# Performance work log

Measured on AMD Instinct MI355X. Metric: run time of the kernel, lower is better.

Reference implementation:

```python
import jax, jax.numpy as jnp
import numpy as np

B, L, D, FF = 4, 4096, 1024, 4096
EPS = 1e-06


def setup_inputs() -> dict:
    key = jax.random.key(0)
    ks = jax.random.split(key, 20)
    s_d = 1.0 / np.sqrt(D)
    s_ff = 1.0 / np.sqrt(FF)
    inp = {
        "x": jax.random.normal(ks[0], (B, L, D), jnp.float32),
        "hidden": jax.random.normal(ks[1], (B, D), jnp.float32),
        # sioconv linears (stored as [in, out])
        "w_ln_z": jax.random.normal(ks[2], (D, D), jnp.float32) * s_d,
        "b_ln_z": jnp.zeros((D,), jnp.float32),
        "w_dt": jax.random.normal(ks[3], (D, D), jnp.float32) * s_d,
        "b_dt": jnp.zeros((D,), jnp.float32),
        "w_y": jax.random.normal(ks[4], (D, D), jnp.float32) * s_d,
        "b_y": jnp.zeros((D,), jnp.float32),
        "w_y_act": jax.random.normal(ks[5], (D, D), jnp.float32) * s_d,
        "b_y_act": jnp.zeros((D,), jnp.float32),
        # FFN SwiGLU
        "w_fc": jax.random.normal(ks[6], (D, FF), jnp.float32) * s_d,
        "b_fc": jnp.zeros((FF,), jnp.float32),
        "w_fc_act": jax.random.normal(ks[7], (D, FF), jnp.float32) * s_d,
        "b_fc_act": jnp.zeros((FF,), jnp.float32),
        "w_out": jax.random.normal(ks[8], (FF, D), jnp.float32) * s_ff,
        "b_out": jnp.zeros((D,), jnp.float32),
        # RMSNorm gains
        "g_sio": jnp.ones((D,), jnp.float32),
        "g_ffn": jnp.ones((D,), jnp.float32),
    }
    return inp


def _rmsnorm(x, g):
    return x * jax.lax.rsqrt(jnp.mean(x * x, axis=-1, keepdims=True) + EPS) * g


def _sioconv(x, hidden, w_ln_z, b_ln_z, w_dt, b_dt, w_y, b_y, w_y_act, b_y_act):
    # x: [B,L,D], hidden: [B,D]
    ln_z = -jax.nn.softplus(-(x @ w_ln_z + b_ln_z))       # [B,L,D]
    dt = x @ w_dt + b_dt
    ln_da = -jax.nn.softplus(-dt)
    ln_o_da = -jax.nn.softplus(dt)
    ln_o_da_cumsum = jnp.cumsum(ln_o_da, axis=1)
    # inner-chunk: exp(logcumsumexp(ln_z + ln_da - cumsum) + cumsum)
    lse = jax.lax.cumlogsumexp(ln_z + ln_da - ln_o_da_cumsum, axis=1)
    h_inner = jnp.exp(lse + ln_o_da_cumsum)
    # cross-chunk: decay applied to incoming hidden state
    h_cross = jnp.exp(ln_o_da_cumsum) * hidden[:, None, :]
    h = h_inner + h_cross
    y = (h @ w_y + b_y) * jax.nn.silu(x @ w_y_act + b_y_act)
    return y, h


def _ffn(x, w_fc, b_fc, w_fc_act, b_fc_act, w_out, b_out):
    return (x @ w_fc + b_fc) * jax.nn.silu(x @ w_fc_act + b_fc_act) @ w_out + b_out


def reference(x, hidden, w_ln_z, b_ln_z, w_dt, b_dt, w_y, b_y, w_y_act, b_y_act,
              w_fc, b_fc, w_fc_act, b_fc_act, w_out, b_out, g_sio, g_ffn):
    x_res = x
    y, h = _sioconv(_rmsnorm(x, g_sio), hidden,
                    w_ln_z, b_ln_z, w_dt, b_dt, w_y, b_y, w_y_act, b_y_act)
    x = y + x_res  # dropout is identity (p=0 / eval)
    x_res = x
    x = _ffn(_rmsnorm(x, g_ffn), w_fc, b_fc, w_fc_act, b_fc_act, w_out, b_out) + x_res
    return (x, h)
```

## Files before the change

kernel.cpp:

```cpp
#include <hip/hip_runtime.h>
#include <stdint.h>

using u16 = unsigned short;
typedef __attribute__((ext_vector_type(8))) __bf16 bf16x8;
typedef __attribute__((ext_vector_type(4))) float f32x4;

#define DEV __device__ __forceinline__

static constexpr int kB = 4, kL = 4096, kD = 1024, kFF = 4096;
static constexpr int kM = kB * kL;
static constexpr int kLC = 256, kNC = kL / kLC;
static constexpr float kEPS = 1e-6f;

DEV u16 f2bf(float v) {
  union { float f; uint32_t u; } x; x.f = v;
  uint32_t r = x.u + 0x7FFFu + ((x.u >> 16) & 1u);
  return (u16)(r >> 16);
}
DEV float bf2f(u16 u) {
  union { uint32_t u; float f; } x; x.u = (uint32_t)u << 16; return x.f;
}
DEV float sigm(float x) { return 1.0f / (1.0f + __expf(-x)); }

DEV void gload_lds16(const void* g, void* l) {
  __builtin_amdgcn_global_load_lds(
      (const __attribute__((address_space(1))) void*)g,
      (__attribute__((address_space(3))) void*)l, 16, 0, 0);
}

__global__ __launch_bounds__(256) void wtrans_all(
    const float* __restrict__ w_ln_z, const float* __restrict__ w_dt,
    const float* __restrict__ w_fca, const float* __restrict__ w_fc,
    const float* __restrict__ w_yact, const float* __restrict__ w_y,
    const float* __restrict__ w_out_,
    u16* __restrict__ wzdT, u16* __restrict__ wfgT, u16* __restrict__ wyaT,
    u16* __restrict__ wyT, u16* __restrict__ woutT) {
  const int bid = blockIdx.x;
  const float *a, *b; u16* out; int K, Ncols, bx, local; bool pair;
  if (bid < 2048)       { local = bid;         a = w_ln_z; b = w_dt; out = wzdT;  K = 1024; Ncols = 1024; bx = 64;  pair = true;  }
  else if (bid < 10240) { local = bid - 2048;  a = w_fca;  b = w_fc; out = wfgT;  K = 1024; Ncols = 4096; bx = 256; pair = true;  }
  else if (bid < 11264) { local = bid - 10240; a = w_yact; b = nullptr; out = wyaT; K = 1024; Ncols = 1024; bx = 32; pair = false; }
  else if (bid < 12288) { local = bid - 11264; a = w_y;    b = nullptr; out = wyT;  K = 1024; Ncols = 1024; bx = 32; pair = false; }
  else                  { local = bid - 12288; a = w_out_; b = nullptr; out = woutT; K = 4096; Ncols = 1024; bx = 32; pair = false; }
  const int n0 = (local % bx) * 32, k0 = (local / bx) * 32;
  __shared__ float t[32][33];
  const int tx = threadIdx.x, ty = threadIdx.y;
  const float* src; int c0;
  if (pair) { src = ((n0 >> 5) & 1) ? b : a; c0 = (n0 >> 6) * 32; }
  else      { src = a; c0 = n0; }
#pragma unroll
  for (int i = 0; i < 4; ++i)
    t[ty + i * 8][tx] = src[(size_t)(k0 + ty + i * 8) * Ncols + (c0 + tx)];
  __syncthreads();
#pragma unroll
  for (int i = 0; i < 4; ++i)
    out[(size_t)(n0 + ty + i * 8) * K + (k0 + tx)] = f2bf(t[tx][ty + i * 8]);
}

__global__ __launch_bounds__(256) void rmsnorm_kernel(const float* __restrict__ x,
                                                      const float* __restrict__ g,
                                                      u16* __restrict__ out) {
  const int row = blockIdx.x;
  const int t = threadIdx.x;
  const float4 v = ((const float4*)(x + (size_t)row * kD))[t];
  float ss = v.x * v.x + v.y * v.y + v.z * v.z + v.w * v.w;
#pragma unroll
  for (int o = 1; o < 64; o <<= 1) ss += __shfl_xor(ss, o, 64);
  __shared__ float red[4];
  if ((t & 63) == 0) red[t >> 6] = ss;
  __syncthreads();
  const float tot = red[0] + red[1] + red[2] + red[3];
  const float sc = rsqrtf(tot * (1.0f / kD) + kEPS);
  const float4 gv = ((const float4*)g)[t];
  const uint32_t lo = (uint32_t)f2bf(v.x * sc * gv.x) | ((uint32_t)f2bf(v.y * sc * gv.y) << 16);
  const uint32_t hi = (uint32_t)f2bf(v.z * sc * gv.z) | ((uint32_t)f2bf(v.w * sc * gv.w) << 16);
  *(uint2*)(out + (size_t)row * kD + t * 4) = make_uint2(lo, hi);
}

template <int MODE>
__global__ __launch_bounds__(512) void gemm256(
    const u16* __restrict__ A, const u16* __restrict__ Bt,
    const float* __restrict__ bias, const float* __restrict__ bias2,
    const u16* __restrict__ aux, int auxld,
    const float* __restrict__ res, float* __restrict__ Cf,
    u16* __restrict__ Cb, u16* __restrict__ C2b,
    int M, int N, int K) {
  __shared__ u16 sm[65536];
  const int tid = threadIdx.x;
  const int lane = tid & 63;
  const int wave = tid >> 6;
  const int wr = wave >> 2, wc = wave & 3;

  const int gx = gridDim.x;
  const int nwg = gx * gridDim.y;
  const int bid = blockIdx.y * gx + blockIdx.x;
  const int q = nwg >> 3, r = nwg & 7;
  const int xcd = bid & 7, idx0 = bid >> 3;
  const int wg = (xcd < r ? xcd * (q + 1) : r * (q + 1) + (xcd - r) * q) + idx0;
  const int m0 = (wg / gx) * 256, n0 = (wg % gx) * 256;

  const int NK = K >> 6;

  const int l8 = lane >> 3, l7 = lane & 7;
  const int rsub = wave * 8 + l8;
  const int kel = (l7 ^ l8) * 8;
  const size_t srcA = (size_t)(m0 + rsub) * K + kel;
  const size_t srcB = (size_t)(n0 + rsub) * K + kel;

  auto stage_half = [&](int kt, int half) {
    const int bsel = (kt & 1) * 32768;
    if (half < 2) {
      u16* d = sm + bsel + tid * 8 + half * 8192;
      const u16* s = A + srcA + (size_t)kt * 64 + (size_t)(half * 2) * 64 * K;
      gload_lds16(s, d);
      gload_lds16(s + (size_t)64 * K, d + 4096);
    } else {
      const int hh = half - 2;
      u16* d = sm + bsel + 16384 + tid * 8 + hh * 8192;
      const u16* s = Bt + srcB + (size_t)kt * 64 + (size_t)(hh * 2) * 64 * K;
      gload_lds16(s, d);
      gload_lds16(s + (size_t)64 * K, d + 4096);
    }
  };

  const int ra = lane & 15;
  const int kx0 = ((lane >> 4) ^ l7) * 8;
  const int kx1 = (((lane >> 4) + 4) ^ l7) * 8;

  f32x4 acc[8][4] = {};
  bf16x8 al[4][2], ah[4][2], bl[2][2], bh[2][2];

  stage_half(0, 0); stage_half(0, 1); stage_half(0, 2); stage_half(0, 3);
  stage_half(1, 0);
  asm volatile("s_waitcnt vmcnt(2)");
  asm volatile("s_barrier" ::: "memory");

  for (int h = 0; h < NK; ++h) {
    const u16* as = sm + (h & 1) * 32768 + (wr * 128 + ra) * 64;
    const u16* bs = sm + (h & 1) * 32768 + 16384 + (wc * 64 + ra) * 64;

#pragma unroll
    for (int mi = 0; mi < 4; ++mi) {
      al[mi][0] = *(const bf16x8*)(as + mi * 16 * 64 + kx0);
      al[mi][1] = *(const bf16x8*)(as + mi * 16 * 64 + kx1);
    }
#pragma unroll
    for (int ni = 0; ni < 2; ++ni) {
      bl[ni][0] = *(const bf16x8*)(bs + ni * 16 * 64 + kx0);
      bl[ni][1] = *(const bf16x8*)(bs + ni * 16 * 64 + kx1);
    }
    if (h + 1 < NK) stage_half(h + 1, 1);
    asm volatile("s_barrier" ::: "memory");
    asm volatile("s_waitcnt lgkmcnt(0)");
    __builtin_amdgcn_s_setprio(1);
#pragma unroll
    for (int mi = 0; mi < 4; ++mi)
#pragma unroll
      for (int ni = 0; ni < 2; ++ni)
#pragma unroll
        for (int kk = 0; kk < 2; ++kk)
          acc[mi][ni] = __builtin_amdgcn_mfma_f32_16x16x32_bf16(al[mi][kk], bl[ni][kk], acc[mi][ni], 0, 0, 0);
    __builtin_amdgcn_s_setprio(0);
    asm volatile("s_barrier" ::: "memory");

#pragma unroll
    for (int ni = 0; ni < 2; ++ni) {
      bh[ni][0] = *(const bf16x8*)(bs + (32 + ni * 16) * 64 + kx0);
      bh[ni][1] = *(const bf16x8*)(bs + (32 + ni * 16) * 64 + kx1);
    }
    if (h + 1 < NK) stage_half(h + 1, 2);
    asm volatile("s_barrier" ::: "memory");
    asm volatile("s_waitcnt lgkmcnt(0)");
    __builtin_amdgcn_s_setprio(1);
#pragma unroll
    for (int mi = 0; mi < 4; ++mi)
#pragma unroll
      for (int ni = 0; ni < 2; ++ni)
#pragma unroll
        for (int kk = 0; kk < 2; ++kk)
          acc[mi][2 + ni] = __builtin_amdgcn_mfma_f32_16x16x32_bf16(al[mi][kk], bh[ni][kk], acc[mi][2 + ni], 0, 0, 0);
    __builtin_amdgcn_s_setprio(0);
    asm volatile("s_barrier" ::: "memory");

#pragma unroll
    for (int mi = 0; mi < 4; ++mi) {
      ah[mi][0] = *(const bf16x8*)(as + (64 + mi * 16) * 64 + kx0);
      ah[mi][1] = *(const bf16x8*)(as + (64 + mi * 16) * 64 + kx1);
    }
    if (h + 1 < NK) stage_half(h + 1, 3);
    asm volatile("s_barrier" ::: "memory");
    asm volatile("s_waitcnt lgkmcnt(0)");
    __builtin_amdgcn_s_setprio(1);
#pragma unroll
    for (int mi = 0; mi < 4; ++mi)
#pragma unroll
      for (int ni = 0; ni < 2; ++ni)
#pragma unroll
        for (int kk = 0; kk < 2; ++kk)
          acc[4 + mi][ni] = __builtin_amdgcn_mfma_f32_16x16x32_bf16(ah[mi][kk], bl[ni][kk], acc[4 + mi][ni], 0, 0, 0);
    __builtin_amdgcn_s_setprio(0);
    asm volatile("s_barrier" ::: "memory");

    if (h + 2 < NK) stage_half(h + 2, 0);
    asm volatile("s_barrier" ::: "memory");
    __builtin_amdgcn_s_setprio(1);
#pragma unroll
    for (int mi = 0; mi < 4; ++mi)
#pragma unroll
      for (int ni = 0; ni < 2; ++ni)
#pragma unroll
        for (int kk = 0; kk < 2; ++kk)
          acc[4 + mi][2 + ni] = __builtin_amdgcn_mfma_f32_16x16x32_bf16(ah[mi][kk], bh[ni][kk], acc[4 + mi][2 + ni], 0, 0, 0);
    __builtin_amdgcn_s_setprio(0);
    if (h + 2 < NK) asm volatile("s_waitcnt vmcnt(2)");
    else            asm volatile("s_waitcnt vmcnt(0)");
    asm volatile("s_barrier" ::: "memory");
  }

  const int ca = ra;
  const int rq = (lane >> 4) * 4;
  if (MODE == 7) {
    const int Nout = N >> 1;
#pragma unroll
    for (int mi = 0; mi < 8; ++mi) {
#pragma unroll
      for (int ni = 0; ni < 2; ++ni) {
        const int cout = (n0 >> 1) + wc * 32 + ni * 16 + ca;
        const float b1 = bias[cout], b2 = bias2[cout];
#pragma unroll
        for (int j = 0; j < 4; ++j) {
          const int rr = m0 + wr * 128 + mi * 16 + rq + j;
          const size_t idx = (size_t)rr * Nout + cout;
          const float v1 = acc[mi][ni][j] + b1;
          const float v2 = acc[mi][2 + ni][j] + b2;
          Cf[idx] = sigm(-v2);
          C2b[idx] = f2bf(sigm(v1) * sigm(v2));
        }
      }
    }
  } else {
#pragma unroll
    for (int mi = 0; mi < 8; ++mi) {
#pragma unroll
      for (int ni = 0; ni < 4; ++ni) {
        const int c = n0 + wc * 64 + ni * 16 + ca;
        const float bz = bias[c];
#pragma unroll
        for (int j = 0; j < 4; ++j) {
          const int rr = m0 + wr * 128 + mi * 16 + rq + j;
          const size_t idx = (size_t)rr * N + c;
          const float v = acc[mi][ni][j] + bz;
          if (MODE == 2) {
            const float a = bf2f(aux[(size_t)rr * auxld + c]);
            Cf[idx] = v * (a * sigm(a)) + res[idx];
          } else if (MODE == 4) {
            Cf[idx] = v + res[idx];
          } else {
            Cb[idx] = f2bf(v);
          }
        }
      }
    }
  }
}

__global__ __launch_bounds__(512, 4) void gemm_ffn(
    const u16* __restrict__ A, const u16* __restrict__ Bt,
    const float* __restrict__ bias, const float* __restrict__ bias2,
    u16* __restrict__ Cb, int M, int N, int K) {
  __shared__ u16 sm[24576];
  const int tid = threadIdx.x;
  const int lane = tid & 63;
  const int wave = tid >> 6;
  const int wr = wave >> 1, wc = wave & 1;

  const int gx = gridDim.x;
  const int nwg = gx * gridDim.y;
  const int bid = blockIdx.y * gx + blockIdx.x;
  const int q = nwg >> 3, r = nwg & 7;
  const int xcd = bid & 7, idx0 = bid >> 3;
  const int wg = (xcd < r ? xcd * (q + 1) : r * (q + 1) + (xcd - r) * q) + idx0;
  const int per = gridDim.y * 4;
  const int sg = wg / per, srem = wg % per;
  const int m0 = (srem >> 2) * 256;
  const int n0 = (sg * 4 + (srem & 3)) * 128;

  const int NK = K >> 5;

  const int rsub = wave * 16 + (lane >> 2);
  const int kel = ((lane & 3) ^ ((lane >> 3) & 3)) * 8;
  const size_t srcA = (size_t)(m0 + rsub) * K + kel;
  const size_t srcB = (size_t)(n0 + rsub) * K + kel;

  auto stageA = [&](int kt) {
    u16* d = sm + (kt & 1) * 12288 + tid * 8;
    const u16* s = A + srcA + (size_t)kt * 32;
    gload_lds16(s, d);
    gload_lds16(s + (size_t)128 * K, d + 4096);
  };
  auto stageB = [&](int kt) {
    gload_lds16(Bt + srcB + (size_t)kt * 32,
                sm + (kt & 1) * 12288 + 8192 + tid * 8);
  };

  const int ra = lane & 15;
  const int rb = ra * 32 + ((((lane >> 4) ^ (ra >> 1)) & 3) << 3);

  f32x4 acc[4][4] = {};
  bf16x8 af[4], bfr[4];

  stageA(0); stageB(0);
  if (NK > 1) { stageA(1); stageB(1); }
  asm volatile("s_waitcnt vmcnt(3)");
  asm volatile("s_barrier" ::: "memory");

  for (int h = 0; h < NK; ++h) {
    const u16* Az = sm + (h & 1) * 12288 + wr * 2048;
    const u16* Bz = sm + (h & 1) * 12288 + 8192 + wc * 2048;

#pragma unroll
    for (int mi = 0; mi < 4; ++mi) af[mi] = *(const bf16x8*)(Az + mi * 512 + rb);
    bfr[0] = *(const bf16x8*)(Bz + rb);
    bfr[1] = *(const bf16x8*)(Bz + 512 + rb);
    asm volatile("s_barrier" ::: "memory");
    asm volatile("s_waitcnt lgkmcnt(0)");
    __builtin_amdgcn_s_setprio(1);
#pragma unroll
    for (int mi = 0; mi < 4; ++mi)
#pragma unroll
      for (int ni = 0; ni < 2; ++ni)
        acc[mi][ni] = __builtin_amdgcn_mfma_f32_16x16x32_bf16(af[mi], bfr[ni], acc[mi][ni], 0, 0, 0);
    __builtin_amdgcn_s_setprio(0);
    asm volatile("s_barrier" ::: "memory");

    bfr[2] = *(const bf16x8*)(Bz + 1024 + rb);
    bfr[3] = *(const bf16x8*)(Bz + 1536 + rb);
    if (h + 2 < NK) stageA(h + 2);
    asm volatile("s_barrier" ::: "memory");
    asm volatile("s_waitcnt lgkmcnt(0)");
    __builtin_amdgcn_s_setprio(1);
#pragma unroll
    for (int mi = 0; mi < 4; ++mi)
      acc[mi][2] = __builtin_amdgcn_mfma_f32_16x16x32_bf16(af[mi], bfr[2], acc[mi][2], 0, 0, 0);
    __builtin_amdgcn_s_setprio(0);
    asm volatile("s_barrier" ::: "memory");

    if (h + 2 < NK) stageB(h + 2);
    __builtin_amdgcn_s_setprio(1);
#pragma unroll
    for (int mi = 0; mi < 4; ++mi)
      acc[mi][3] = __builtin_amdgcn_mfma_f32_16x16x32_bf16(af[mi], bfr[3], acc[mi][3], 0, 0, 0);
    __builtin_amdgcn_s_setprio(0);
    if (h + 2 < NK) asm volatile("s_waitcnt vmcnt(3)");
    else            asm volatile("s_waitcnt vmcnt(0)");
    asm volatile("s_barrier" ::: "memory");
  }

  const int ca = lane & 15;
  const int rq = (lane >> 4) * 4;
  const int Nout = N >> 1;
#pragma unroll
  for (int mi = 0; mi < 4; ++mi) {
#pragma unroll
    for (int ni = 0; ni < 2; ++ni) {
      const int cout = (n0 >> 1) + wc * 32 + ni * 16 + ca;
      const float b1 = bias[cout], b2 = bias2[cout];
#pragma unroll
      for (int j = 0; j < 4; ++j) {
        const int rr = m0 + wr * 64 + mi * 16 + rq + j;
        const size_t idx = (size_t)rr * Nout + cout;
        const float v1 = acc[mi][ni][j] + b1;
        const float v2 = acc[mi][2 + ni][j] + b2;
        Cb[idx] = f2bf(v2 * (v1 * sigm(v1)));
      }
    }
  }
}

__global__ __launch_bounds__(256) void scan_phase1(const float* __restrict__ Aa,
                                                   const u16* __restrict__ Bv,
                                                   float* __restrict__ P,
                                                   float* __restrict__ S) {
  const int d = blockIdx.x * 256 + threadIdx.x;
  const int c = blockIdx.y, b = blockIdx.z;
  size_t base = ((size_t)b * kL + (size_t)c * kLC) * kD + d;
  float p = 1.0f, s = 0.0f;
#pragma unroll 4
  for (int l = 0; l < kLC; ++l) {
    const float a = Aa[base];
    const float bv = bf2f(Bv[base]);
    p *= a;
    s = fmaf(a, s, bv);
    base += kD;
  }
  const size_t o = ((size_t)b * kNC + c) * kD + d;
  P[o] = p; S[o] = s;
}

__global__ __launch_bounds__(256) void scan_phase2(const float* __restrict__ P,
                                                   const float* __restrict__ S,
                                                   const float* __restrict__ hidden,
                                                   float* __restrict__ Hini) {
  const int d = blockIdx.x * 256 + threadIdx.x;
  const int b = blockIdx.y;
  float carry = hidden[(size_t)b * kD + d];
  for (int c = 0; c < kNC; ++c) {
    const size_t o = ((size_t)b * kNC + c) * kD + d;
    Hini[o] = carry;
    carry = fmaf(P[o], carry, S[o]);
  }
}

__global__ __launch_bounds__(256) void scan_phase3(const float* __restrict__ Aa,
                                                   const u16* __restrict__ Bv,
                                                   const float* __restrict__ Hini,
                                                   float* __restrict__ Hout,
                                                   u16* __restrict__ Hbf) {
  const int d = blockIdx.x * 256 + threadIdx.x;
  const int c = blockIdx.y, b = blockIdx.z;
  float h = Hini[((size_t)b * kNC + c) * kD + d];
  size_t base = ((size_t)b * kL + (size_t)c * kLC) * kD + d;
#pragma unroll 4
  for (int l = 0; l < kLC; ++l) {
    h = fmaf(Aa[base], h, bf2f(Bv[base]));
    Hout[base] = h;
    Hbf[base] = f2bf(h);
    base += kD;
  }
}

extern "C" void kernel_launch(void* const* d_in, const int* in_sizes, int n_in,
                              void* d_out, int out_size, void* d_ws, size_t ws_size,
                              hipStream_t stream) {
  const float* x      = (const float*)d_in[0];
  const float* hidden = (const float*)d_in[1];
  const float* w_ln_z = (const float*)d_in[2];
  const float* b_ln_z = (const float*)d_in[3];
  const float* w_dt   = (const float*)d_in[4];
  const float* b_dt   = (const float*)d_in[5];
  const float* w_y    = (const float*)d_in[6];
  const float* b_y    = (const float*)d_in[7];
  const float* w_yact = (const float*)d_in[8];
  const float* b_yact = (const float*)d_in[9];
  const float* w_fc   = (const float*)d_in[10];
  const float* b_fc   = (const float*)d_in[11];
  const float* w_fca  = (const float*)d_in[12];
  const float* b_fca  = (const float*)d_in[13];
  const float* w_out  = (const float*)d_in[14];
  const float* b_out  = (const float*)d_in[15];
  const float* g_sio  = (const float*)d_in[16];
  const float* g_ffn  = (const float*)d_in[17];

  char* ws = (char*)d_ws;
  const size_t MiB = 1ull << 20;
  u16* wzdT  = (u16*)(ws + 0 * MiB);
  u16* wyaT  = (u16*)(ws + 4 * MiB);
  u16* wyT   = (u16*)(ws + 6 * MiB);
  u16* wfgT  = (u16*)(ws + 8 * MiB);
  u16* woutT = (u16*)(ws + 24 * MiB);
  u16*   xn    = (u16*)(ws + 33 * MiB);
  u16*   yabuf = (u16*)(ws + 65 * MiB);
  float* Abuf  = (float*)(ws + 97 * MiB);
  u16*   Bvbuf = (u16*)(ws + 161 * MiB);
  u16*   hbf   = (u16*)(ws + 225 * MiB);
  u16*   Ubuf  = (u16*)(ws + 161 * MiB);
  float* Pbuf  = (float*)(ws + 289 * MiB);
  float* Sbuf  = (float*)(ws + 290 * MiB);
  float* Hini  = (float*)(ws + 291 * MiB);

  float* xout = (float*)d_out;
  float* hout = xout + (size_t)kM * kD;
  float* x1 = Abuf;

  wtrans_all<<<16384, dim3(32, 8), 0, stream>>>(
      w_ln_z, w_dt, w_fca, w_fc, w_yact, w_y, w_out,
      wzdT, wfgT, wyaT, wyT, woutT);

  rmsnorm_kernel<<<kM, 256, 0, stream>>>(x, g_sio, xn);

  gemm256<7><<<dim3(2048 / 256, kM / 256), 512, 0, stream>>>(
      xn, wzdT, b_ln_z, b_dt, nullptr, 0, nullptr, Abuf, nullptr, Bvbuf, kM, 2048, kD);
  gemm256<5><<<dim3(kD / 256, kM / 256), 512, 0, stream>>>(
      xn, wyaT, b_yact, nullptr, nullptr, 0, nullptr, nullptr, yabuf, nullptr, kM, kD, kD);

  scan_phase1<<<dim3(kD / 256, kNC, kB), 256, 0, stream>>>(Abuf, Bvbuf, Pbuf, Sbuf);
  scan_phase2<<<dim3(kD / 256, kB), 256, 0, stream>>>(Pbuf, Sbuf, hidden, Hini);
  scan_phase3<<<dim3(kD / 256, kNC, kB), 256, 0, stream>>>(Abuf, Bvbuf, Hini, hout, hbf);

  gemm256<2><<<dim3(kD / 256, kM / 256), 512, 0, stream>>>(
      hbf, wyT, b_y, nullptr, yabuf, kD, x, x1, nullptr, nullptr, kM, kD, kD);

  rmsnorm_kernel<<<kM, 256, 0, stream>>>(x1, g_ffn, xn);

  gemm_ffn<<<dim3(8192 / 128, kM / 256), 512, 0, stream>>>(
      xn, wfgT, b_fca, b_fc, Ubuf, kM, 8192, kD);

  gemm256<4><<<dim3(kD / 256, kM / 256), 512, 0, stream>>>(
      Ubuf, woutT, b_out, nullptr, nullptr, 0, x1, xout, nullptr, nullptr, kM, kD, kFF);
}
```

Baseline: 732.5 us.

## Fuse scan chunk reduction into gate GEMM epilogue and store residual in bf16

The per-chunk product/sum reduction of the scan (scan_phase1) now runs inside the MODE 7 GEMM epilogue, using shuffles and shared memory across the 256-row tile, so the separate pass that re-read the A and B buffers is gone. Separately, the intermediate residual x1 is written as bf16 instead of fp32. The second RMSNorm and the final output GEMM read that bf16 copy, which cuts memory traffic. The cost is lower precision on the residual path and a longer GEMM epilogue. The fused reduction also relies on each 256-row tile lining up exactly with one scan chunk.

```diff
diff --git a/kernel.cpp b/kernel.cpp
--- a/kernel.cpp
+++ b/kernel.cpp
@@ -77,6 +77,28 @@
   *(uint2*)(out + (size_t)row * kD + t * 4) = make_uint2(lo, hi);
 }
 
+__global__ __launch_bounds__(256) void rmsnorm_b16(const u16* __restrict__ x,
+                                                   const float* __restrict__ g,
+                                                   u16* __restrict__ out) {
+  const int row = blockIdx.x;
+  const int t = threadIdx.x;
+  const uint2 raw = ((const uint2*)(x + (size_t)row * kD))[t];
+  const float v0 = bf2f((u16)(raw.x & 0xffff)), v1 = bf2f((u16)(raw.x >> 16));
+  const float v2 = bf2f((u16)(raw.y & 0xffff)), v3 = bf2f((u16)(raw.y >> 16));
+  float ss = v0 * v0 + v1 * v1 + v2 * v2 + v3 * v3;
+#pragma unroll
+  for (int o = 1; o < 64; o <<= 1) ss += __shfl_xor(ss, o, 64);
+  __shared__ float red[4];
+  if ((t & 63) == 0) red[t >> 6] = ss;
+  __syncthreads();
+  const float tot = red[0] + red[1] + red[2] + red[3];
+  const float sc = rsqrtf(tot * (1.0f / kD) + kEPS);
+  const float4 gv = ((const float4*)g)[t];
+  const uint32_t lo = (uint32_t)f2bf(v0 * sc * gv.x) | ((uint32_t)f2bf(v1 * sc * gv.y) << 16);
+  const uint32_t hi = (uint32_t)f2bf(v2 * sc * gv.z) | ((uint32_t)f2bf(v3 * sc * gv.w) << 16);
+  *(uint2*)(out + (size_t)row * kD + t * 4) = make_uint2(lo, hi);
+}
+
 template <int MODE>
 __global__ __launch_bounds__(512) void gemm256(
     const u16* __restrict__ A, const u16* __restrict__ Bt,
@@ -84,6 +106,7 @@
     const u16* __restrict__ aux, int auxld,
     const float* __restrict__ res, float* __restrict__ Cf,
     u16* __restrict__ Cb, u16* __restrict__ C2b,
+    float* __restrict__ Pg, float* __restrict__ Sg,
     int M, int N, int K) {
   __shared__ u16 sm[65536];
   const int tid = threadIdx.x;
@@ -221,21 +244,60 @@
   const int rq = (lane >> 4) * 4;
   if (MODE == 7) {
     const int Nout = N >> 1;
+    float Pacc[2] = {1.f, 1.f}, Sacc[2] = {0.f, 0.f};
 #pragma unroll
     for (int mi = 0; mi < 8; ++mi) {
 #pragma unroll
       for (int ni = 0; ni < 2; ++ni) {
         const int cout = (n0 >> 1) + wc * 32 + ni * 16 + ca;
         const float b1 = bias[cout], b2 = bias2[cout];
+        float pj = 1.f, sj = 0.f;
 #pragma unroll
         for (int j = 0; j < 4; ++j) {
           const int rr = m0 + wr * 128 + mi * 16 + rq + j;
           const size_t idx = (size_t)rr * Nout + cout;
           const float v1 = acc[mi][ni][j] + b1;
           const float v2 = acc[mi][2 + ni][j] + b2;
-          Cf[idx] = sigm(-v2);
-          C2b[idx] = f2bf(sigm(v1) * sigm(v2));
+          const float Aa = sigm(-v2);
+          const float Bb = sigm(v1) * sigm(v2);
+          Cf[idx] = Aa;
+          C2b[idx] = f2bf(Bb);
+          pj *= Aa;
+          sj = fmaf(Aa, sj, Bb);
         }
+        float P16 = 1.f, S16 = 0.f;
+#pragma unroll
+        for (int qq = 0; qq < 4; ++qq) {
+          const float pq = __shfl(pj, ca + qq * 16, 64);
+          const float sq = __shfl(sj, ca + qq * 16, 64);
+          P16 *= pq;
+          S16 = fmaf(pq, S16, sq);
+        }
+        Sacc[ni] = fmaf(P16, Sacc[ni], S16);
+        Pacc[ni] *= P16;
+      }
+    }
+    float* smF = (float*)sm;
+    __syncthreads();
+    if ((lane >> 4) == 0) {
+#pragma unroll
+      for (int ni = 0; ni < 2; ++ni) {
+        const int col = wc * 32 + ni * 16 + ca;
+        smF[wr * 128 + col] = Pacc[ni];
+        smF[256 + wr * 128 + col] = Sacc[ni];
+      }
+    }
+    __syncthreads();
+    if (wr == 0 && (lane >> 4) == 0) {
+      const int bb = m0 >> 12, cc = (m0 & 4095) >> 8;
+#pragma unroll
+      for (int ni = 0; ni < 2; ++ni) {
+        const int col = wc * 32 + ni * 16 + ca;
+        const float P0 = smF[col],       P1 = smF[128 + col];
+        const float S0 = smF[256 + col], S1 = smF[256 + 128 + col];
+        const size_t o = ((size_t)bb * kNC + cc) * kD + ((n0 >> 1) + col);
+        Pg[o] = P0 * P1;
+        Sg[o] = fmaf(P1, S0, S1);
       }
     }
   } else {
@@ -252,9 +314,9 @@
           const float v = acc[mi][ni][j] + bz;
           if (MODE == 2) {
             const float a = bf2f(aux[(size_t)rr * auxld + c]);
-            Cf[idx] = v * (a * sigm(a)) + res[idx];
-          } else if (MODE == 4) {
-            Cf[idx] = v + res[idx];
+            Cb[idx] = f2bf(v * (a * sigm(a)) + res[idx]);
+          } else if (MODE == 8) {
+            Cf[idx] = v + bf2f(aux[(size_t)rr * auxld + c]);
           } else {
             Cb[idx] = f2bf(v);
           }
@@ -375,26 +437,6 @@
       }
     }
   }
-}
-
-__global__ __launch_bounds__(256) void scan_phase1(const float* __restrict__ Aa,
-                                                   const u16* __restrict__ Bv,
-                                                   float* __restrict__ P,
-                                                   float* __restrict__ S) {
-  const int d = blockIdx.x * 256 + threadIdx.x;
-  const int c = blockIdx.y, b = blockIdx.z;
-  size_t base = ((size_t)b * kL + (size_t)c * kLC) * kD + d;
-  float p = 1.0f, s = 0.0f;
-#pragma unroll 4
-  for (int l = 0; l < kLC; ++l) {
-    const float a = Aa[base];
-    const float bv = bf2f(Bv[base]);
-    p *= a;
-    s = fmaf(a, s, bv);
-    base += kD;
-  }
-  const size_t o = ((size_t)b * kNC + c) * kD + d;
-  P[o] = p; S[o] = s;
 }
 
 __global__ __launch_bounds__(256) void scan_phase2(const float* __restrict__ P,
@@ -461,6 +503,7 @@
   u16*   xn    = (u16*)(ws + 33 * MiB);
   u16*   yabuf = (u16*)(ws + 65 * MiB);
   float* Abuf  = (float*)(ws + 97 * MiB);
+  u16*   x1b   = (u16*)(ws + 97 * MiB);
   u16*   Bvbuf = (u16*)(ws + 161 * MiB);
   u16*   hbf   = (u16*)(ws + 225 * MiB);
   u16*   Ubuf  = (u16*)(ws + 161 * MiB);
@@ -470,7 +513,6 @@
 
   float* xout = (float*)d_out;
   float* hout = xout + (size_t)kM * kD;
-  float* x1 = Abuf;
 
   wtrans_all<<<16384, dim3(32, 8), 0, stream>>>(
       w_ln_z, w_dt, w_fca, w_fc, w_yact, w_y, w_out,
@@ -479,22 +521,25 @@
   rmsnorm_kernel<<<kM, 256, 0, stream>>>(x, g_sio, xn);
 
   gemm256<7><<<dim3(2048 / 256, kM / 256), 512, 0, stream>>>(
-      xn, wzdT, b_ln_z, b_dt, nullptr, 0, nullptr, Abuf, nullptr, Bvbuf, kM, 2048, kD);
+      xn, wzdT, b_ln_z, b_dt, nullptr, 0, nullptr, Abuf, nullptr, Bvbuf,
+      Pbuf, Sbuf, kM, 2048, kD);
   gemm256<5><<<dim3(kD / 256, kM / 256), 512, 0, stream>>>(
-      xn, wyaT, b_yact, nullptr, nullptr, 0, nullptr, nullptr, yabuf, nullptr, kM, kD, kD);
-
-  scan_phase1<<<dim3(kD / 256, kNC, kB), 256, 0, stream>>>(Abuf, Bvbuf, Pbuf, Sbuf);
+      xn, wyaT, b_yact, nullptr, nullptr, 0, nullptr, nullptr, yabuf, nullptr,
+      nullptr, nullptr, kM, kD, kD);
+
   scan_phase2<<<dim3(kD / 256, kB), 256, 0, stream>>>(Pbuf, Sbuf, hidden, Hini);
   scan_phase3<<<dim3(kD / 256, kNC, kB), 256, 0, stream>>>(Abuf, Bvbuf, Hini, hout, hbf);
 
   gemm256<2><<<dim3(kD / 256, kM / 256), 512, 0, stream>>>(
-      hbf, wyT, b_y, nullptr, yabuf, kD, x, x1, nullptr, nullptr, kM, kD, kD);
-
-  rmsnorm_kernel<<<kM, 256, 0, stream>>>(x1, g_ffn, xn);
+      hbf, wyT, b_y, nullptr, yabuf, kD, x, nullptr, x1b, nullptr,
+      nullptr, nullptr, kM, kD, kD);
+
+  rmsnorm_b16<<<kM, 256, 0, stream>>>(x1b, g_ffn, xn);
 
   gemm_ffn<<<dim3(8192 / 128, kM / 256), 512, 0, stream>>>(
       xn, wfgT, b_fca, b_fc, Ubuf, kM, 8192, kD);
 
-  gemm256<4><<<dim3(kD / 256, kM / 256), 512, 0, stream>>>(
-      Ubuf, woutT, b_out, nullptr, nullptr, 0, x1, xout, nullptr, nullptr, kM, kD, kFF);
-}
+  gemm256<8><<<dim3(kD / 256, kM / 256), 512, 0, stream>>>(
+      Ubuf, woutT, b_out, nullptr, x1b, kD, nullptr, xout, nullptr, nullptr,
+      nullptr, nullptr, kM, kD, kFF);
+}
```

New measurement: 730.6 us (median of 2 runs). Within noise of the previous version (-0.3%).
